# Optimization experiments

Measured on AMD Instinct MI355X. Metric: run time of the kernel, lower is better.

## Reference

```python
import jax, jax.numpy as jnp
import numpy as np
import math

D_MODEL = 512
SLOPE = 0.5  # slope_init, not trainable


def setup_inputs() -> dict:
    key = jax.random.key(0)
    k1, k2, k3, k4 = jax.random.split(key, 4)
    B, S, D = 4, 4096, D_MODEL
    x = jax.random.normal(k1, (B, S, D), dtype=jnp.float32)
    # nn.Linear(d, d): weight is [d, d]; query_key weight used as x @ W (no transpose, bias unused)
    lim = 1.0 / math.sqrt(D)
    W_qk = jax.random.uniform(k2, (D, D), jnp.float32, -lim, lim)
    W_v = jax.random.uniform(k3, (D, D), jnp.float32, -lim, lim)
    b_v = jax.random.uniform(k4, (D,), jnp.float32, -lim, lim)
    return {"x": x, "W_qk": W_qk, "W_v": W_v, "b_v": b_v}


def reference(x, W_qk, W_v, b_v):
    B, S, D = x.shape
    scale = 1.0 / math.sqrt(D)
    # scores[b,i,j] = (x @ W_qk @ x^T) * scale   (torch: x @ weight @ x.transpose)
    scores = jnp.einsum('bid,de,bje->bij', x, W_qk, x) * scale
    # ALiBi bias: (j - i) * slope
    i = jnp.arange(S, dtype=x.dtype)[:, None]
    j = jnp.arange(S, dtype=x.dtype)[None, :]
    scores = scores + (j - i) * jnp.asarray(SLOPE, x.dtype)
    # causal mask: strict upper triangle -> -inf
    causal = j > i  # [S, S] bool
    scores = jnp.where(causal, -jnp.inf, scores)
    attn = jax.nn.softmax(scores, axis=-1)
    # value_linear: x @ W_v^T + b_v (standard nn.Linear)
    v = jnp.einsum('bjd,ed->bje', x, W_v) + b_v
    return jnp.einsum('bij,bje->bie', attn, v)
```

## Files before the change

### kernel.cpp

```cpp
#include <hip/hip_runtime.h>
#include <math.h>

#define D_MODEL 512
#define SEQ     4096
#define BATCH   4
#define BS      (BATCH * SEQ)

typedef __attribute__((ext_vector_type(8))) short  short8;
typedef __attribute__((ext_vector_type(4))) float  float4v;

#define GAS __attribute__((address_space(1)))
#define LAS __attribute__((address_space(3)))

__device__ __forceinline__ void gld_lds16(const void* g, void* l) {
  __builtin_amdgcn_global_load_lds((const GAS unsigned int*)g,
                                   (LAS unsigned int*)l, 16, 0, 0);
}

__device__ __forceinline__ unsigned short bf16r(float f) {
  unsigned int u = __builtin_bit_cast(unsigned int, f);
  u += 0x7fffu + ((u >> 16) & 1u);
  return (unsigned short)(u >> 16);
}

__device__ __forceinline__ uint4 pack8(float4 a, float4 b) {
  uint4 o;
  o.x = bf16r(a.x) | ((unsigned)bf16r(a.y) << 16);
  o.y = bf16r(a.z) | ((unsigned)bf16r(a.w) << 16);
  o.z = bf16r(b.x) | ((unsigned)bf16r(b.y) << 16);
  o.w = bf16r(b.z) | ((unsigned)bf16r(b.w) << 16);
  return o;
}

__global__ __launch_bounds__(256) void cvt_w(const float* __restrict__ Wqk,
                                             unsigned short* __restrict__ Wqkt,
                                             const float* __restrict__ Wv,
                                             unsigned short* __restrict__ Wvb) {
  if (blockIdx.x < 64) {
    __shared__ float tile[64][65];
    const int bx = blockIdx.x & 7;
    const int by = blockIdx.x >> 3;
    const int tx = threadIdx.x & 63;
    const int ty = threadIdx.x >> 6;
    for (int r = ty; r < 64; r += 4)
      tile[r][tx] = Wqk[(size_t)(by * 64 + r) * D_MODEL + bx * 64 + tx];
    __syncthreads();
    for (int r = ty; r < 64; r += 4)
      Wqkt[(size_t)(bx * 64 + r) * D_MODEL + by * 64 + tx] = bf16r(tile[tx][r]);
  } else {
    const int idx = ((blockIdx.x - 64) * 256 + threadIdx.x) * 8;
    const float4 a = *(const float4*)(Wv + idx);
    const float4 b = *(const float4*)(Wv + idx + 4);
    *(uint4*)(Wvb + idx) = pack8(a, b);
  }
}

template <bool VT>
__device__ __forceinline__ void gemm_path(const float* __restrict__ x,
                                          const unsigned short* __restrict__ Wgt,
                                          const float* __restrict__ bias,
                                          unsigned short* __restrict__ xb,
                                          unsigned short* __restrict__ C,
                                          int a0, float alpha,
                                          unsigned short* Ws, unsigned short* As) {
  const int t    = threadIdx.x;
  const int w    = t >> 6;
  const int lane = t & 63;
  const int q    = lane >> 4;
  const int c    = lane & 15;
  const int wbase = w * 128;

  const int arow = t >> 2;
  const int acb  = (t & 3) * 16;

  constexpr int NI = VT ? 8 : 4;
  constexpr int NJ = VT ? 4 : 8;

  float4v acc[NI][NJ];
#pragma unroll
  for (int i = 0; i < NI; ++i)
#pragma unroll
    for (int j = 0; j < NJ; ++j) acc[i][j] = (float4v){0.f, 0.f, 0.f, 0.f};

  for (int k0 = 0; k0 < D_MODEL; k0 += 64) {
#pragma unroll
    for (int it = 0; it < 16; ++it) {
      const int idx = it * 256 + t;
      gld_lds16(Wgt + (size_t)(idx >> 3) * D_MODEL + k0 + (idx & 7) * 8,
                &Ws[idx * 8]);
    }
    {
      const float* xg = x + (size_t)(a0 + arow) * D_MODEL + k0 + acb;
      const float4 f0 = *(const float4*)(xg + 0);
      const float4 f1 = *(const float4*)(xg + 4);
      const float4 f2 = *(const float4*)(xg + 8);
      const float4 f3 = *(const float4*)(xg + 12);
      const uint4 u0 = pack8(f0, f1);
      const uint4 u1 = pack8(f2, f3);
      *(uint4*)&As[arow * 64 + acb]     = u0;
      *(uint4*)&As[arow * 64 + acb + 8] = u1;
      if (!VT) {
        unsigned short* xo = xb + (size_t)(a0 + arow) * D_MODEL + k0 + acb;
        *(uint4*)xo       = u0;
        *(uint4*)(xo + 8) = u1;
      }
    }
    __syncthreads();

#pragma unroll
    for (int kc = 0; kc < 2; ++kc) {
      short8 af[NI], bf[NJ];
#pragma unroll
      for (int i = 0; i < NI; ++i) {
        const unsigned short* src = VT ? &Ws[(wbase + i * 16 + c) * 64 + kc * 32 + q * 8]
                                       : &As[(i * 16 + c) * 64 + kc * 32 + q * 8];
        af[i] = *(const short8*)src;
      }
#pragma unroll
      for (int j = 0; j < NJ; ++j) {
        const unsigned short* src = VT ? &As[(j * 16 + c) * 64 + kc * 32 + q * 8]
                                       : &Ws[(wbase + j * 16 + c) * 64 + kc * 32 + q * 8];
        bf[j] = *(const short8*)src;
      }
#pragma unroll
      for (int i = 0; i < NI; ++i)
#pragma unroll
        for (int j = 0; j < NJ; ++j)
          acc[i][j] = __builtin_amdgcn_mfma_f32_16x16x32_bf16(af[i], bf[j], acc[i][j], 0, 0, 0);
    }
    __syncthreads();
  }

  if (!VT) {
#pragma unroll
    for (int i = 0; i < NI; ++i)
#pragma unroll
      for (int tt = 0; tt < 4; ++tt) {
        const int row = a0 + i * 16 + 4 * q + tt;
#pragma unroll
        for (int j = 0; j < NJ; ++j)
          C[(size_t)row * D_MODEL + wbase + j * 16 + c] = bf16r(alpha * acc[i][j][tt]);
      }
  } else {
#pragma unroll
    for (int i = 0; i < NI; ++i)
#pragma unroll
      for (int tt = 0; tt < 4; ++tt) {
        const int dim = wbase + i * 16 + 4 * q + tt;
        const float bv = bias[dim];
#pragma unroll
        for (int j = 0; j < NJ; ++j)
          C[(size_t)dim * BS + a0 + j * 16 + c] = bf16r(acc[i][j][tt] + bv);
      }
  }
}

__global__ __launch_bounds__(256, 2) void qv_gemm(const float* __restrict__ x,
                                                  const unsigned short* __restrict__ Wqkt,
                                                  const unsigned short* __restrict__ Wvb,
                                                  const float* __restrict__ bv,
                                                  unsigned short* __restrict__ xb,
                                                  unsigned short* __restrict__ Qb,
                                                  unsigned short* __restrict__ Vt,
                                                  float scale) {
  __shared__ unsigned short Ws[512 * 64];
  __shared__ unsigned short As[64 * 64];
  if (blockIdx.x < 256)
    gemm_path<false>(x, Wqkt, nullptr, xb, Qb, blockIdx.x * 64, scale, Ws, As);
  else
    gemm_path<true>(x, Wvb, bv, nullptr, Vt, (blockIdx.x - 256) * 64, 1.0f, Ws, As);
}

__global__ __launch_bounds__(128) void attn_tile(const unsigned short* __restrict__ Q,
                                                 const unsigned short* __restrict__ Kx,
                                                 const unsigned short* __restrict__ Vt,
                                                 float* __restrict__ out) {
  constexpr int PLD = 72;
  __shared__ unsigned short pls[16 * PLD];
  __shared__ float lm[2][16], ls[2][16];

  const int t    = threadIdx.x;
  const int h    = t >> 6;
  const int lane = t & 63;
  const int q    = lane >> 4;
  const int c    = lane & 15;

  const int tile = ((blockIdx.x & 7) << 7) + (blockIdx.x >> 3);
  const int r0   = tile << 4;
  const int b    = r0 >> 12;
  const int i0   = r0 & (SEQ - 1);
  const int jb   = i0 - 48;

  short8 qf[16];
  {
    const unsigned short* qp = Q + (size_t)(r0 + c) * D_MODEL + q * 8;
#pragma unroll
    for (int ch = 0; ch < 16; ++ch) qf[ch] = *(const short8*)(qp + ch * 32);
  }

  float4v sacc[2];
  sacc[0] = (float4v){0.f, 0.f, 0.f, 0.f};
  sacc[1] = (float4v){0.f, 0.f, 0.f, 0.f};
#pragma unroll
  for (int s = 0; s < 2; ++s) {
    const int sj = 2 * h + s;
    if (jb + 16 * sj + 15 < 0) continue;
    int krow = jb + 16 * sj + c;
    if (krow < 0) krow = 0;
    const unsigned short* kr = Kx + ((size_t)(b << 12) + krow) * D_MODEL + q * 8;
    float4v sv = sacc[s];
#pragma unroll
    for (int ch = 0; ch < 16; ++ch)
      sv = __builtin_amdgcn_mfma_f32_16x16x32_bf16(qf[ch], *(const short8*)(kr + ch * 32), sv, 0, 0, 0);
    sacc[s] = sv;
  }

  float tmax[4] = {-1e30f, -1e30f, -1e30f, -1e30f};
#pragma unroll
  for (int s = 0; s < 2; ++s)
#pragma unroll
    for (int tt = 0; tt < 4; ++tt) {
      const int jl = jb + 16 * (2 * h + s) + c;
      const int il = i0 + 4 * q + tt;
      float sv = sacc[s][tt];
      sv = (jl < 0 || jl > il) ? -1e30f : sv + 0.5f * (float)(jl - il);
      sacc[s][tt] = sv;
      tmax[tt] = fmaxf(tmax[tt], sv);
    }
#pragma unroll
  for (int tt = 0; tt < 4; ++tt) {
    float v = tmax[tt];
    v = fmaxf(v, __shfl_xor(v, 1, 64));
    v = fmaxf(v, __shfl_xor(v, 2, 64));
    v = fmaxf(v, __shfl_xor(v, 4, 64));
    v = fmaxf(v, __shfl_xor(v, 8, 64));
    tmax[tt] = v;
  }
  if (c == 0) {
#pragma unroll
    for (int tt = 0; tt < 4; ++tt) lm[h][4 * q + tt] = tmax[tt];
  }
  __syncthreads();

  float m[4];
#pragma unroll
  for (int tt = 0; tt < 4; ++tt)
    m[tt] = fmaxf(lm[0][4 * q + tt], lm[1][4 * q + tt]);

  float rsum[4] = {0.f, 0.f, 0.f, 0.f};
#pragma unroll
  for (int s = 0; s < 2; ++s)
#pragma unroll
    for (int tt = 0; tt < 4; ++tt) {
      const float p = __expf(sacc[s][tt] - m[tt]);
      rsum[tt] += p;
      pls[(4 * q + tt) * PLD + (2 * h + s) * 16 + c] = bf16r(p);
    }
#pragma unroll
  for (int tt = 0; tt < 4; ++tt) {
    float v = rsum[tt];
    v += __shfl_xor(v, 1, 64);
    v += __shfl_xor(v, 2, 64);
    v += __shfl_xor(v, 4, 64);
    v += __shfl_xor(v, 8, 64);
    rsum[tt] = v;
  }
  if (c == 0) {
#pragma unroll
    for (int tt = 0; tt < 4; ++tt) ls[h][4 * q + tt] = rsum[tt];
  }
  __syncthreads();

  float l[4];
#pragma unroll
  for (int tt = 0; tt < 4; ++tt)
    l[tt] = ls[0][4 * q + tt] + ls[1][4 * q + tt];

  float4v oacc[16];
#pragma unroll
  for (int dt = 0; dt < 16; ++dt) oacc[dt] = (float4v){0.f, 0.f, 0.f, 0.f};

#pragma unroll
  for (int c2 = 0; c2 < 2; ++c2) {
    if (jb + 32 * c2 + 31 < 0) continue;
    const short8 pa = *(const short8*)&pls[c * PLD + c2 * 32 + q * 8];
    int kk = jb + c2 * 32 + q * 8;
    if (kk < 0) kk = 0;
    const unsigned short* vb = Vt + (size_t)(h * 256 + c) * BS + (b << 12) + kk;
#pragma unroll
    for (int dt = 0; dt < 16; ++dt) {
      const short8 vf = *(const short8*)(vb + (size_t)dt * 16 * BS);
      oacc[dt] = __builtin_amdgcn_mfma_f32_16x16x32_bf16(pa, vf, oacc[dt], 0, 0, 0);
    }
  }

  float inv[4];
#pragma unroll
  for (int tt = 0; tt < 4; ++tt) inv[tt] = 1.0f / l[tt];
#pragma unroll
  for (int dt = 0; dt < 16; ++dt)
#pragma unroll
    for (int tt = 0; tt < 4; ++tt)
      out[(size_t)(r0 + 4 * q + tt) * D_MODEL + h * 256 + dt * 16 + c] =
          oacc[dt][tt] * inv[tt];
}

extern "C" void kernel_launch(void* const* d_in, const int* in_sizes, int n_in,
                              void* d_out, int out_size, void* d_ws,
                              size_t ws_size, hipStream_t stream) {
  const float* x   = (const float*)d_in[0];
  const float* Wqk = (const float*)d_in[1];
  const float* Wv  = (const float*)d_in[2];
  const float* bv  = (const float*)d_in[3];
  float* out = (float*)d_out;

  unsigned short* xb   = (unsigned short*)d_ws;
  unsigned short* Qb   = xb + (size_t)BS * D_MODEL;
  unsigned short* Vt   = Qb + (size_t)BS * D_MODEL;
  unsigned short* Wqkt = Vt + (size_t)BS * D_MODEL;
  unsigned short* Wvb  = Wqkt + (size_t)D_MODEL * D_MODEL;

  const float scale = 1.0f / sqrtf((float)D_MODEL);

  cvt_w<<<dim3(192), dim3(256), 0, stream>>>(Wqk, Wqkt, Wv, Wvb);
  qv_gemm<<<dim3(512), dim3(256), 0, stream>>>(x, Wqkt, Wvb, bv, xb, Qb, Vt, scale);
  attn_tile<<<dim3(BS / 16), dim3(128), 0, stream>>>(Qb, xb, Vt, out);
}
```

Baseline: 139.4 us.

## Drop bf16 copy of x; read fp32 x directly in attention and swizzle GEMM blocks

Removes the bf16 xb side output written by the Q GEMM. The attention kernel now loads keys straight from the fp32 input x and converts them to bf16 in registers before each MFMA. This saves a full-size write and workspace buffer, but the key reads in attention now move twice as many bytes and add conversion instructions. It also remaps GEMM block indices with an interleaving swizzle, which is meant to change how blocks are spread across the GPU or improve cache locality.

```diff
diff --git a/kernel.cpp b/kernel.cpp
--- a/kernel.cpp
+++ b/kernel.cpp
@@ -59,7 +59,6 @@
 __device__ __forceinline__ void gemm_path(const float* __restrict__ x,
                                           const unsigned short* __restrict__ Wgt,
                                           const float* __restrict__ bias,
-                                          unsigned short* __restrict__ xb,
                                           unsigned short* __restrict__ C,
                                           int a0, float alpha,
                                           unsigned short* Ws, unsigned short* As) {
@@ -95,15 +94,8 @@
       const float4 f1 = *(const float4*)(xg + 4);
       const float4 f2 = *(const float4*)(xg + 8);
       const float4 f3 = *(const float4*)(xg + 12);
-      const uint4 u0 = pack8(f0, f1);
-      const uint4 u1 = pack8(f2, f3);
-      *(uint4*)&As[arow * 64 + acb]     = u0;
-      *(uint4*)&As[arow * 64 + acb + 8] = u1;
-      if (!VT) {
-        unsigned short* xo = xb + (size_t)(a0 + arow) * D_MODEL + k0 + acb;
-        *(uint4*)xo       = u0;
-        *(uint4*)(xo + 8) = u1;
-      }
+      *(uint4*)&As[arow * 64 + acb]     = pack8(f0, f1);
+      *(uint4*)&As[arow * 64 + acb + 8] = pack8(f2, f3);
     }
     __syncthreads();
 
@@ -159,20 +151,23 @@
                                                   const unsigned short* __restrict__ Wqkt,
                                                   const unsigned short* __restrict__ Wvb,
                                                   const float* __restrict__ bv,
-                                                  unsigned short* __restrict__ xb,
                                                   unsigned short* __restrict__ Qb,
                                                   unsigned short* __restrict__ Vt,
                                                   float scale) {
   __shared__ unsigned short Ws[512 * 64];
   __shared__ unsigned short As[64 * 64];
-  if (blockIdx.x < 256)
-    gemm_path<false>(x, Wqkt, nullptr, xb, Qb, blockIdx.x * 64, scale, Ws, As);
-  else
-    gemm_path<true>(x, Wvb, bv, nullptr, Vt, (blockIdx.x - 256) * 64, 1.0f, Ws, As);
+  if (blockIdx.x < 256) {
+    const int a0 = (((blockIdx.x & 7) << 5) | (blockIdx.x >> 3)) * 64;
+    gemm_path<false>(x, Wqkt, nullptr, Qb, a0, scale, Ws, As);
+  } else {
+    const int b2 = blockIdx.x - 256;
+    const int a0 = (((b2 & 7) << 5) | (b2 >> 3)) * 64;
+    gemm_path<true>(x, Wvb, bv, Vt, a0, 1.0f, Ws, As);
+  }
 }
 
 __global__ __launch_bounds__(128) void attn_tile(const unsigned short* __restrict__ Q,
-                                                 const unsigned short* __restrict__ Kx,
+                                                 const float* __restrict__ x,
                                                  const unsigned short* __restrict__ Vt,
                                                  float* __restrict__ out) {
   constexpr int PLD = 72;
@@ -207,11 +202,15 @@
     if (jb + 16 * sj + 15 < 0) continue;
     int krow = jb + 16 * sj + c;
     if (krow < 0) krow = 0;
-    const unsigned short* kr = Kx + ((size_t)(b << 12) + krow) * D_MODEL + q * 8;
+    const float* kr = x + ((size_t)(b << 12) + krow) * D_MODEL + q * 8;
     float4v sv = sacc[s];
 #pragma unroll
-    for (int ch = 0; ch < 16; ++ch)
-      sv = __builtin_amdgcn_mfma_f32_16x16x32_bf16(qf[ch], *(const short8*)(kr + ch * 32), sv, 0, 0, 0);
+    for (int ch = 0; ch < 16; ++ch) {
+      const float4 f0 = *(const float4*)(kr + ch * 32);
+      const float4 f1 = *(const float4*)(kr + ch * 32 + 4);
+      const uint4 u = pack8(f0, f1);
+      sv = __builtin_amdgcn_mfma_f32_16x16x32_bf16(qf[ch], __builtin_bit_cast(short8, u), sv, 0, 0, 0);
+    }
     sacc[s] = sv;
   }
 
@@ -314,8 +313,7 @@
   const float* bv  = (const float*)d_in[3];
   float* out = (float*)d_out;
 
-  unsigned short* xb   = (unsigned short*)d_ws;
-  unsigned short* Qb   = xb + (size_t)BS * D_MODEL;
+  unsigned short* Qb   = (unsigned short*)d_ws;
   unsigned short* Vt   = Qb + (size_t)BS * D_MODEL;
   unsigned short* Wqkt = Vt + (size_t)BS * D_MODEL;
   unsigned short* Wvb  = Wqkt + (size_t)D_MODEL * D_MODEL;
@@ -323,6 +321,6 @@
   const float scale = 1.0f / sqrtf((float)D_MODEL);
 
   cvt_w<<<dim3(192), dim3(256), 0, stream>>>(Wqk, Wqkt, Wv, Wvb);
-  qv_gemm<<<dim3(512), dim3(256), 0, stream>>>(x, Wqkt, Wvb, bv, xb, Qb, Vt, scale);
-  attn_tile<<<dim3(BS / 16), dim3(128), 0, stream>>>(Qb, xb, Vt, out);
-}
+  qv_gemm<<<dim3(512), dim3(256), 0, stream>>>(x, Wqkt, Wvb, bv, Qb, Vt, scale);
+  attn_tile<<<dim3(BS / 16), dim3(128), 0, stream>>>(Qb, x, Vt, out);
+}
```

New measurement: 142.8 us. 1.02x slower.
